# Performance work log

Measured on AMD Instinct MI355X. Metric: run time of the kernel, lower is better.

## Reference

```python
import jax, jax.numpy as jnp
import numpy as np

B, S, H = 2, 2048, 2048
NH, NKV, HD = 16, 4, 128
ROPE_BASE = 10000.0


def rotate_half(x):
    x1, x2 = jnp.split(x, 2, axis=-1)
    return jnp.concatenate((-x2, x1), axis=-1)


def setup_inputs() -> dict:
    key = jax.random.key(0)
    ks = jax.random.split(key, 6)
    hidden_states = jax.random.normal(ks[0], (B, S, H), dtype=jnp.float32)
    # additive causal mask, as used by HF: 0 on allowed, large negative on masked
    causal = jnp.triu(jnp.full((S, S), -1e9, dtype=jnp.float32), k=1)
    attention_mask = jnp.broadcast_to(causal[None, None], (B, 1, S, S))
    position_ids = jnp.broadcast_to(jnp.arange(S, dtype=jnp.int64)[None], (B, S))
    scale = 1.0 / np.sqrt(H)
    Wq = jax.random.normal(ks[1], (NH * HD, H), dtype=jnp.float32) * scale
    Wk = jax.random.normal(ks[2], (NKV * HD, H), dtype=jnp.float32) * scale
    Wv = jax.random.normal(ks[3], (NKV * HD, H), dtype=jnp.float32) * scale
    Wo = jax.random.normal(ks[4], (H, NH * HD), dtype=jnp.float32) * scale
    return {"hidden_states": hidden_states, "attention_mask": attention_mask,
            "position_ids": position_ids, "Wq": Wq, "Wk": Wk, "Wv": Wv, "Wo": Wo}


def reference(hidden_states, attention_mask, position_ids, Wq, Wk, Wv, Wo):
    b, s, _ = hidden_states.shape
    # projections (torch Linear: y = x W^T)
    q = jnp.einsum('bsh,oh->bso', hidden_states, Wq).reshape(b, s, NH, HD).transpose(0, 2, 1, 3)
    k = jnp.einsum('bsh,oh->bso', hidden_states, Wk).reshape(b, s, NKV, HD).transpose(0, 2, 1, 3)
    v = jnp.einsum('bsh,oh->bso', hidden_states, Wv).reshape(b, s, NKV, HD).transpose(0, 2, 1, 3)
    # RoPE
    inv_freq = 1.0 / (ROPE_BASE ** (jnp.arange(0, HD, 2, dtype=jnp.float32) / HD))  # [HD/2]
    freqs = position_ids.astype(jnp.float32)[:, :, None] * inv_freq[None, None, :]  # [B,S,HD/2]
    emb = jnp.concatenate((freqs, freqs), axis=-1)                                  # [B,S,HD]
    cos = jnp.cos(emb)[:, None]  # [B,1,S,HD]
    sin = jnp.sin(emb)[:, None]
    q = q * cos + rotate_half(q) * sin
    k = k * cos + rotate_half(k) * sin
    # GQA repeat (repeat_interleave along head axis)
    n_rep = NH // NKV
    k = jnp.repeat(k, n_rep, axis=1)
    v = jnp.repeat(v, n_rep, axis=1)
    scale = HD ** -0.5
    attn = jnp.einsum('bhqd,bhkd->bhqk', q, k) * scale
    attn = attn + attention_mask
    attn = jax.nn.softmax(attn.astype(jnp.float32), axis=-1).astype(q.dtype)
    out = jnp.einsum('bhqk,bhkd->bhqd', attn, v)            # [B,NH,S,HD]
    out = out.transpose(0, 2, 1, 3).reshape(b, s, NH * HD)  # [B,S,H]
    return jnp.einsum('bso,ho->bsh', out, Wo)
```

## Files before the change

kernel.cpp:

```cpp
#include <hip/hip_runtime.h>


#define B_ 2
#define S_ 2048
#define H_ 2048
#define NH_ 16
#define NKV_ 4
#define HD_ 128
#define QKV_N 3072

typedef unsigned short u16;
typedef unsigned int u32;
typedef unsigned long long u64;
typedef __attribute__((ext_vector_type(8))) short short8;
typedef __attribute__((ext_vector_type(4))) float floatx4;
typedef __attribute__((ext_vector_type(16))) float floatx16;

__device__ __forceinline__ u16 f2bf(float f) {
    union { float f; u32 u; } v; v.f = f;
    u32 u = v.u;
    return (u16)((u + 0x7fffu + ((u >> 16) & 1u)) >> 16);
}
__device__ __forceinline__ float bf2f(u16 h) {
    union { u32 u; float f; } v; v.u = ((u32)h) << 16;
    return v.f;
}
__device__ __forceinline__ void store_out(u16* p, float v)  { *p = f2bf(v); }
__device__ __forceinline__ void store_out(float* p, float v) { *p = v; }

__device__ __forceinline__ void gload_lds16(const void* g, void* l) {
    __builtin_amdgcn_global_load_lds(
        (const __attribute__((address_space(1))) void*)g,
        (__attribute__((address_space(3))) void*)l, 16, 0, 0);
}

__device__ __forceinline__ u32 cvtpk(float lo, float hi) {
    u32 r;
    asm("v_cvt_pk_bf16_f32 %0, %1, %2" : "=v"(r) : "v"(lo), "v"(hi));
    return r;
}

__device__ __forceinline__ void pl32swap(u32& a, u32& b) {
#if __has_builtin(__builtin_amdgcn_permlane32_swap)
    typedef __attribute__((ext_vector_type(2))) int iv2;
    iv2 r = __builtin_amdgcn_permlane32_swap((int)a, (int)b, false, false);
    a = (u32)r[0];
    b = (u32)r[1];
#else
    asm volatile("v_permlane32_swap_b32 %0, %1" : "+v"(a), "+v"(b));
#endif
}

__global__ __launch_bounds__(256) void cast_all(const float* __restrict__ hs,
                                                const float* __restrict__ Wq,
                                                const float* __restrict__ Wk,
                                                const float* __restrict__ Wv,
                                                const float* __restrict__ Wo,
                                                u16* __restrict__ hs_b,
                                                u16* __restrict__ wqkv_b,
                                                u16* __restrict__ wo_b) {
    int q = blockIdx.x * 256 + threadIdx.x;
    const float* src;
    u16* dst;
    if (q < 2097152)      { src = hs; dst = hs_b; }
    else if (q < 3145728) { q -= 2097152; src = Wq; dst = wqkv_b; }
    else if (q < 3407872) { q -= 3145728; src = Wk; dst = wqkv_b + 2048 * 2048; }
    else if (q < 3670016) { q -= 3407872; src = Wv; dst = wqkv_b + 2560 * 2048; }
    else                  { q -= 3670016; src = Wo; dst = wo_b; }
    float4 f = ((const float4*)src)[q];
    u32 lo = ((u32)f2bf(f.y) << 16) | f2bf(f.x);
    u32 hi2 = ((u32)f2bf(f.w) << 16) | f2bf(f.z);
    *(u64*)(dst + (size_t)q * 4) = (u64)lo | ((u64)hi2 << 32);
}

template <typename OutT>
__global__ __launch_bounds__(256) void gemm128(const u16* __restrict__ A,
                                               const u16* __restrict__ Bm,
                                               OutT* __restrict__ C,
                                               int M, int N, int K) {
    __shared__ __align__(16) u16 As[128][32];
    __shared__ __align__(16) u16 Bs[128][32];
    const int tid  = threadIdx.x;
    const int wave = tid >> 6;
    const int lane = tid & 63;
    const int quad = lane >> 4;
    const int l16  = lane & 15;

    const int nbx = gridDim.x, nby = gridDim.y;
    const int total = nbx * nby;
    int n = (int)blockIdx.y * nbx + (int)blockIdx.x;
    if ((total & 7) == 0) {
        int cpx = total >> 3;
        n = (n & 7) * cpx + (n >> 3);
    }
    const int m0 = (n / nbx) * 128;
    const int n0 = (n % nbx) * 128;

    const int wm = (wave >> 1) * 64;
    const int wn = (wave & 1) * 64;
    const int srow = tid >> 2;
    const int scol = (tid & 3) * 8;

    floatx4 acc[4][4] = {};

    for (int k0 = 0; k0 < K; k0 += 32) {
        __syncthreads();
        gload_lds16(A  + (size_t)(m0 + srow) * K + k0 + scol,      &As[srow][scol]);
        gload_lds16(A  + (size_t)(m0 + 64 + srow) * K + k0 + scol, &As[64 + srow][scol]);
        gload_lds16(Bm + (size_t)(n0 + srow) * K + k0 + scol,      &Bs[srow][scol]);
        gload_lds16(Bm + (size_t)(n0 + 64 + srow) * K + k0 + scol, &Bs[64 + srow][scol]);
        __syncthreads();
        short8 af[4], bfv[4];
        for (int i = 0; i < 4; ++i) {
            af[i]  = *(const short8*)&As[wm + i * 16 + l16][quad * 8];
            bfv[i] = *(const short8*)&Bs[wn + i * 16 + l16][quad * 8];
        }
        for (int mi = 0; mi < 4; ++mi)
            for (int ni = 0; ni < 4; ++ni)
                acc[mi][ni] = __builtin_amdgcn_mfma_f32_16x16x32_bf16(
                    af[mi], bfv[ni], acc[mi][ni], 0, 0, 0);
    }
    for (int mi = 0; mi < 4; ++mi)
        for (int ni = 0; ni < 4; ++ni)
            for (int r = 0; r < 4; ++r) {
                int row = m0 + wm + mi * 16 + quad * 4 + r;
                int col = n0 + wn + ni * 16 + l16;
                store_out(C + (size_t)row * N + col, acc[mi][ni][r]);
            }
}

__global__ __launch_bounds__(256) void rope2(u16* buf) {
    int i = blockIdx.x * 256 + threadIdx.x;
    int hofs, nheads;
    float oscale;
    if (i < 4194304) { hofs = 0;    nheads = 16; oscale = 0.08838834764831845f; }
    else             { i -= 4194304; hofs = 2048; nheads = 4;  oscale = 1.0f; }
    int d = i & 63;
    int t = i >> 6;
    int head = t % nheads;
    int row  = t / nheads;
    int s    = row & (S_ - 1);
    size_t base = (size_t)row * QKV_N + hofs + head * HD_;
    float invf = exp2f(-(float)d * (13.28771237954945f / 64.0f));
    float fr = (float)s * invf;
    float sn, cs;
    sincosf(fr, &sn, &cs);
    float x1 = bf2f(buf[base + d]);
    float x2 = bf2f(buf[base + d + 64]);
    buf[base + d]      = f2bf((x1 * cs - x2 * sn) * oscale);
    buf[base + d + 64] = f2bf((x2 * cs + x1 * sn) * oscale);
}

__global__ __launch_bounds__(256) void transpose_v(const u16* __restrict__ qkv,
                                                   u16* __restrict__ vt) {
    __shared__ u16 t[32][33];
    const int tx = threadIdx.x, ty = threadIdx.y;
    const int c0 = blockIdx.x * 32, s0 = blockIdx.y * 32, b = blockIdx.z;
    for (int i = 0; i < 4; ++i)
        t[ty + i * 8][tx] =
            qkv[((size_t)(b * S_ + s0 + ty + i * 8)) * QKV_N + 2560 + c0 + tx];
    __syncthreads();
    for (int i = 0; i < 4; ++i)
        vt[((size_t)(b * 512 + c0 + ty + i * 8)) * S_ + s0 + tx] = t[tx][ty + i * 8];
}

__global__ __launch_bounds__(256) void flash_attn(const u16* __restrict__ qkv,
                                                  const u16* __restrict__ vtg,
                                                  u16* __restrict__ o) {
    __shared__ __align__(16) u16 KsL[64 * 128];
    __shared__ __align__(16) u16 VtL[128 * 64];

    const int tid  = threadIdx.x;
    const int wave = tid >> 6;
    const int lane = tid & 63;
    const int l31  = lane & 31;
    const int hi   = lane >> 5;
    const int wq   = wave >> 1;
    const int kb   = wave & 1;

    const int bx = (int)blockIdx.x;
    const int by = (int)blockIdx.y;
    const int flip = (by >> 3) & 1;
    const int a4 = bx & 15;
    const int jq = flip ? a4 : (31 - a4);
    const int bh = (by & 7) | (((by >> 4) & 1) << 3) | ((bx >> 4) << 4);
    const int b   = bh >> 4;
    const int h   = bh & 15;
    const int kvh = h >> 2;
    const int q0  = jq * 64;

    const size_t qb = ((size_t)(b * S_ + q0 + wq * 32 + l31)) * QKV_N + h * HD_;
    short8 qf[8];
#pragma unroll
    for (int mf = 0; mf < 8; ++mf)
        qf[mf] = *(const short8*)(qkv + qb + mf * 16 + hi * 8);

    floatx16 o_acc[4] = {};
    float l_loc = 0.f;

    const size_t kbase = (size_t)(b * S_) * QKV_N + 2048 + kvh * HD_;
    const size_t vbase = (size_t)((b * NKV_ + kvh) * HD_) * S_;
    const int krow_l = (lane >> 4);
    const int kslot  = lane & 15;
    const int vrow_l = (lane >> 3);
    const int vslot  = lane & 7;

    const int rk = kb * 32 + l31;
    const int kswz = rk & 7;

    for (int kt = 0; kt <= jq; ++kt) {
        __syncthreads();
#pragma unroll
        for (int p = 0; p < 4; ++p) {
            int r = 16 * wave + 4 * p + krow_l;
            gload_lds16(qkv + kbase + (size_t)(kt * 64 + r) * QKV_N
                            + ((kslot ^ (r & 7)) * 8),
                        &KsL[(16 * wave + 4 * p) * 128 + lane * 8]);
            int rv = 32 * wave + 8 * p + vrow_l;
            gload_lds16(vtg + vbase + (size_t)rv * S_ + kt * 64
                            + ((vslot ^ (rv & 7)) * 8),
                        &VtL[(32 * wave + 8 * p) * 64 + lane * 8]);
        }
        __syncthreads();

        floatx16 st = {};
#pragma unroll
        for (int mf = 0; mf < 8; ++mf) {
            short8 kf = *(const short8*)&KsL[rk * 128 + (((mf * 2 + hi) ^ kswz) * 8)];
            st = __builtin_amdgcn_mfma_f32_32x32x16_bf16(kf, qf[mf], st, 0, 0, 0);
        }
        if (kt == jq) {
            int qloc = wq * 32 + l31;
#pragma unroll
            for (int r = 0; r < 16; ++r) {
                int krow = kb * 32 + (r & 3) + 8 * (r >> 2) + 4 * hi;
                if (krow > qloc) st[r] = -INFINITY;
            }
        }
        u32 pk[8];
        float ll = 0.f;
#pragma unroll
        for (int i = 0; i < 8; ++i) {
            float e0 = __expf(st[2 * i]);
            float e1 = __expf(st[2 * i + 1]);
            ll += e0 + e1;
            pk[i] = cvtpk(e0, e1);
        }
        l_loc += ll;
        pl32swap(pk[0], pk[2]);
        pl32swap(pk[1], pk[3]);
        pl32swap(pk[4], pk[6]);
        pl32swap(pk[5], pk[7]);
        union { u32 u[4]; short8 s; } c0, c1;
        c0.u[0] = pk[0]; c0.u[1] = pk[1]; c0.u[2] = pk[2]; c0.u[3] = pk[3];
        c1.u[0] = pk[4]; c1.u[1] = pk[5]; c1.u[2] = pk[6]; c1.u[3] = pk[7];
#pragma unroll
        for (int dblk = 0; dblk < 4; ++dblk) {
            int rv = dblk * 32 + l31;
            int sw = rv & 7;
            short8 va = *(const short8*)&VtL[rv * 64 + (((kb * 4 + hi) ^ sw) * 8)];
            o_acc[dblk] = __builtin_amdgcn_mfma_f32_32x32x16_bf16(va, c0.s, o_acc[dblk], 0, 0, 0);
            short8 vb = *(const short8*)&VtL[rv * 64 + (((kb * 4 + 2 + hi) ^ sw) * 8)];
            o_acc[dblk] = __builtin_amdgcn_mfma_f32_32x32x16_bf16(vb, c1.s, o_acc[dblk], 0, 0, 0);
        }
    }

    float lt = l_loc + __shfl_xor(l_loc, 32, 64);
    __syncthreads();
    float* scr = (float*)KsL;
    if (kb == 1) scr[wq * 64 + lane] = lt;
    __syncthreads();
    float linv = 0.f;
    if (kb == 0) linv = 1.0f / (lt + scr[wq * 64 + lane]);

#pragma unroll
    for (int dblk = 0; dblk < 4; ++dblk) {
        __syncthreads();
        if (kb == 1) {
#pragma unroll
            for (int r = 0; r < 16; ++r)
                scr[wq * 1088 + lane * 17 + r] = o_acc[dblk][r];
        }
        __syncthreads();
        if (kb == 0) {
            const int row = q0 + wq * 32 + l31;
#pragma unroll
            for (int rg = 0; rg < 4; ++rg) {
                float v0 = (o_acc[dblk][rg * 4 + 0] + scr[wq * 1088 + lane * 17 + rg * 4 + 0]) * linv;
                float v1 = (o_acc[dblk][rg * 4 + 1] + scr[wq * 1088 + lane * 17 + rg * 4 + 1]) * linv;
                float v2 = (o_acc[dblk][rg * 4 + 2] + scr[wq * 1088 + lane * 17 + rg * 4 + 2]) * linv;
                float v3 = (o_acc[dblk][rg * 4 + 3] + scr[wq * 1088 + lane * 17 + rg * 4 + 3]) * linv;
                u32 wlo = cvtpk(v0, v1);
                u32 whi = cvtpk(v2, v3);
                int col = h * HD_ + dblk * 32 + rg * 8 + 4 * hi;
                u64 pack = (u64)wlo | ((u64)whi << 32);
                *(u64*)(o + ((size_t)(b * S_ + row)) * H_ + col) = pack;
            }
        }
    }
}

extern "C" void kernel_launch(void* const* d_in, const int* in_sizes, int n_in,
                              void* d_out, int out_size, void* d_ws, size_t ws_size,
                              hipStream_t stream) {
    const float* hs = (const float*)d_in[0];
    const float* Wq = (const float*)d_in[3];
    const float* Wk = (const float*)d_in[4];
    const float* Wv = (const float*)d_in[5];
    const float* Wo = (const float*)d_in[6];

    char* ws = (char*)d_ws;
    const size_t MB = 1024 * 1024;
    u16* hs_b   = (u16*)(ws + 0);
    u16* wqkv_b = (u16*)(ws + 16 * MB);
    u16* vt_b   = (u16*)(ws + 16 * MB);
    u16* wo_b   = (u16*)(ws + 28 * MB);
    u16* qkv    = (u16*)(ws + 36 * MB);

    const int M = B_ * S_;

    cast_all<<<18432, 256, 0, stream>>>(hs, Wq, Wk, Wv, Wo, hs_b, wqkv_b, wo_b);

    gemm128<u16><<<dim3(QKV_N / 128, M / 128), 256, 0, stream>>>(
        hs_b, wqkv_b, qkv, M, QKV_N, H_);

    rope2<<<20480, 256, 0, stream>>>(qkv);

    transpose_v<<<dim3(16, 64, 2), dim3(32, 8), 0, stream>>>(qkv, vt_b);

    flash_attn<<<dim3(32, 32), 256, 0, stream>>>(qkv, vt_b, hs_b);

    gemm128<float><<<dim3(H_ / 128, M / 128), 256, 0, stream>>>(
        hs_b, wo_b, (float*)d_out, M, H_, H_);
}
```

Before: 332.6 us.

## Double the GEMM K-tile and register-prefetch K/V tiles in attention

The GEMM now stages a 64-wide K slice per iteration instead of 32, which halves the number of barrier pairs and gives each wave two MFMA sub-steps per sync. In the attention kernel, K and V tiles are now loaded from global memory into registers one iteration ahead and then written to LDS, replacing the direct global-to-LDS loads. The goal is to overlap global latency with the QK/PV MFMA work. The cost is more LDS in the GEMM and more registers in attention, which may lower occupancy.

```diff
diff --git a/kernel.cpp b/kernel.cpp
--- a/kernel.cpp
+++ b/kernel.cpp
@@ -78,8 +78,8 @@
                                                const u16* __restrict__ Bm,
                                                OutT* __restrict__ C,
                                                int M, int N, int K) {
-    __shared__ __align__(16) u16 As[128][32];
-    __shared__ __align__(16) u16 Bs[128][32];
+    __shared__ __align__(16) u16 As[128][64];
+    __shared__ __align__(16) u16 Bs[128][64];
     const int tid  = threadIdx.x;
     const int wave = tid >> 6;
     const int lane = tid & 63;
@@ -98,30 +98,42 @@
 
     const int wm = (wave >> 1) * 64;
     const int wn = (wave & 1) * 64;
-    const int srow = tid >> 2;
-    const int scol = (tid & 3) * 8;
+    const int srow = tid >> 3;
+    const int scol = (tid & 7) * 8;
 
     floatx4 acc[4][4] = {};
 
-    for (int k0 = 0; k0 < K; k0 += 32) {
-        __syncthreads();
-        gload_lds16(A  + (size_t)(m0 + srow) * K + k0 + scol,      &As[srow][scol]);
-        gload_lds16(A  + (size_t)(m0 + 64 + srow) * K + k0 + scol, &As[64 + srow][scol]);
-        gload_lds16(Bm + (size_t)(n0 + srow) * K + k0 + scol,      &Bs[srow][scol]);
-        gload_lds16(Bm + (size_t)(n0 + 64 + srow) * K + k0 + scol, &Bs[64 + srow][scol]);
-        __syncthreads();
-        short8 af[4], bfv[4];
-        for (int i = 0; i < 4; ++i) {
-            af[i]  = *(const short8*)&As[wm + i * 16 + l16][quad * 8];
-            bfv[i] = *(const short8*)&Bs[wn + i * 16 + l16][quad * 8];
-        }
-        for (int mi = 0; mi < 4; ++mi)
-            for (int ni = 0; ni < 4; ++ni)
-                acc[mi][ni] = __builtin_amdgcn_mfma_f32_16x16x32_bf16(
-                    af[mi], bfv[ni], acc[mi][ni], 0, 0, 0);
-    }
+    for (int k0 = 0; k0 < K; k0 += 64) {
+        __syncthreads();
+#pragma unroll
+        for (int g = 0; g < 4; ++g) {
+            gload_lds16(A  + (size_t)(m0 + g * 32 + srow) * K + k0 + scol,
+                        &As[g * 32 + srow][scol]);
+            gload_lds16(Bm + (size_t)(n0 + g * 32 + srow) * K + k0 + scol,
+                        &Bs[g * 32 + srow][scol]);
+        }
+        __syncthreads();
+#pragma unroll
+        for (int ks = 0; ks < 2; ++ks) {
+            short8 af[4], bfv[4];
+#pragma unroll
+            for (int i = 0; i < 4; ++i) {
+                af[i]  = *(const short8*)&As[wm + i * 16 + l16][ks * 32 + quad * 8];
+                bfv[i] = *(const short8*)&Bs[wn + i * 16 + l16][ks * 32 + quad * 8];
+            }
+#pragma unroll
+            for (int mi = 0; mi < 4; ++mi)
+#pragma unroll
+                for (int ni = 0; ni < 4; ++ni)
+                    acc[mi][ni] = __builtin_amdgcn_mfma_f32_16x16x32_bf16(
+                        af[mi], bfv[ni], acc[mi][ni], 0, 0, 0);
+        }
+    }
+#pragma unroll
     for (int mi = 0; mi < 4; ++mi)
+#pragma unroll
         for (int ni = 0; ni < 4; ++ni)
+#pragma unroll
             for (int r = 0; r < 4; ++r) {
                 int row = m0 + wm + mi * 16 + quad * 4 + r;
                 int col = n0 + wn + ni * 16 + l16;
@@ -204,24 +216,43 @@
     const int kslot  = lane & 15;
     const int vrow_l = (lane >> 3);
     const int vslot  = lane & 7;
+    int kr_[4], kc_[4], vr_[4], vc_[4];
+#pragma unroll
+    for (int p = 0; p < 4; ++p) {
+        kr_[p] = 16 * wave + 4 * p + krow_l;
+        kc_[p] = (kslot ^ (kr_[p] & 7)) * 8;
+        vr_[p] = 32 * wave + 8 * p + vrow_l;
+        vc_[p] = (vslot ^ (vr_[p] & 7)) * 8;
+    }
 
     const int rk = kb * 32 + l31;
     const int kswz = rk & 7;
 
+    short8 kreg[4], vreg[4];
+#pragma unroll
+    for (int p = 0; p < 4; ++p) {
+        kreg[p] = *(const short8*)(qkv + kbase + (size_t)kr_[p] * QKV_N + kc_[p]);
+        vreg[p] = *(const short8*)(vtg + vbase + (size_t)vr_[p] * S_ + vc_[p]);
+    }
+
     for (int kt = 0; kt <= jq; ++kt) {
         __syncthreads();
 #pragma unroll
         for (int p = 0; p < 4; ++p) {
-            int r = 16 * wave + 4 * p + krow_l;
-            gload_lds16(qkv + kbase + (size_t)(kt * 64 + r) * QKV_N
-                            + ((kslot ^ (r & 7)) * 8),
-                        &KsL[(16 * wave + 4 * p) * 128 + lane * 8]);
-            int rv = 32 * wave + 8 * p + vrow_l;
-            gload_lds16(vtg + vbase + (size_t)rv * S_ + kt * 64
-                            + ((vslot ^ (rv & 7)) * 8),
-                        &VtL[(32 * wave + 8 * p) * 64 + lane * 8]);
-        }
-        __syncthreads();
+            *(short8*)&KsL[(16 * wave + 4 * p) * 128 + lane * 8] = kreg[p];
+            *(short8*)&VtL[(32 * wave + 8 * p) * 64 + lane * 8]  = vreg[p];
+        }
+        __syncthreads();
+
+        if (kt < jq) {
+            const size_t ko = kbase + (size_t)((kt + 1) * 64) * QKV_N;
+            const size_t vo = vbase + (size_t)((kt + 1) * 64);
+#pragma unroll
+            for (int p = 0; p < 4; ++p) {
+                kreg[p] = *(const short8*)(qkv + ko + (size_t)kr_[p] * QKV_N + kc_[p]);
+                vreg[p] = *(const short8*)(vtg + vo + (size_t)vr_[p] * S_ + vc_[p]);
+            }
+        }
 
         floatx16 st = {};
 #pragma unroll
```

Result: slower. 367.4 us (+10.5%).

## Register-prefetch next K/V tile in flash attention and fuse rope with V transpose

Applied to the files above, without the earlier changes.

The flash attention loop now loads the next K and V tiles into registers while the current tile is being computed, then writes them to LDS at the start of the next iteration. This replaces the direct global-to-LDS loads and is meant to hide global memory latency behind the MFMA work. Separately, the rope and V-transpose kernels are merged into one launch to save a kernel launch. The merge is safe because the rope blocks only touch the Q and K regions and the transpose blocks only read the V region. The prefetch costs extra registers, which may reduce occupancy.

```diff
diff --git a/kernel.cpp b/kernel.cpp
--- a/kernel.cpp
+++ b/kernel.cpp
@@ -129,39 +129,43 @@
             }
 }
 
-__global__ __launch_bounds__(256) void rope2(u16* buf) {
-    int i = blockIdx.x * 256 + threadIdx.x;
-    int hofs, nheads;
-    float oscale;
-    if (i < 4194304) { hofs = 0;    nheads = 16; oscale = 0.08838834764831845f; }
-    else             { i -= 4194304; hofs = 2048; nheads = 4;  oscale = 1.0f; }
-    int d = i & 63;
-    int t = i >> 6;
-    int head = t % nheads;
-    int row  = t / nheads;
-    int s    = row & (S_ - 1);
-    size_t base = (size_t)row * QKV_N + hofs + head * HD_;
-    float invf = exp2f(-(float)d * (13.28771237954945f / 64.0f));
-    float fr = (float)s * invf;
-    float sn, cs;
-    sincosf(fr, &sn, &cs);
-    float x1 = bf2f(buf[base + d]);
-    float x2 = bf2f(buf[base + d + 64]);
-    buf[base + d]      = f2bf((x1 * cs - x2 * sn) * oscale);
-    buf[base + d + 64] = f2bf((x2 * cs + x1 * sn) * oscale);
-}
-
-__global__ __launch_bounds__(256) void transpose_v(const u16* __restrict__ qkv,
-                                                   u16* __restrict__ vt) {
-    __shared__ u16 t[32][33];
-    const int tx = threadIdx.x, ty = threadIdx.y;
-    const int c0 = blockIdx.x * 32, s0 = blockIdx.y * 32, b = blockIdx.z;
-    for (int i = 0; i < 4; ++i)
-        t[ty + i * 8][tx] =
-            qkv[((size_t)(b * S_ + s0 + ty + i * 8)) * QKV_N + 2560 + c0 + tx];
-    __syncthreads();
-    for (int i = 0; i < 4; ++i)
-        vt[((size_t)(b * 512 + c0 + ty + i * 8)) * S_ + s0 + tx] = t[tx][ty + i * 8];
+__global__ __launch_bounds__(256) void rope_trans(u16* __restrict__ buf,
+                                                  u16* __restrict__ vt) {
+    const int bid = blockIdx.x;
+    const int tid = threadIdx.x;
+    if (bid < 20480) {
+        int i = bid * 256 + tid;
+        int hofs, nheads;
+        float oscale;
+        if (i < 4194304) { hofs = 0;    nheads = 16; oscale = 0.08838834764831845f; }
+        else             { i -= 4194304; hofs = 2048; nheads = 4;  oscale = 1.0f; }
+        int d = i & 63;
+        int t = i >> 6;
+        int head = t % nheads;
+        int row  = t / nheads;
+        int s    = row & (S_ - 1);
+        size_t base = (size_t)row * QKV_N + hofs + head * HD_;
+        float invf = exp2f(-(float)d * (13.28771237954945f / 64.0f));
+        float fr = (float)s * invf;
+        float sn, cs;
+        sincosf(fr, &sn, &cs);
+        float x1 = bf2f(buf[base + d]);
+        float x2 = bf2f(buf[base + d + 64]);
+        buf[base + d]      = f2bf((x1 * cs - x2 * sn) * oscale);
+        buf[base + d + 64] = f2bf((x2 * cs + x1 * sn) * oscale);
+    } else {
+        __shared__ u16 t[32][33];
+        const int b2 = bid - 20480;
+        const int bx = b2 & 15, by = (b2 >> 4) & 63, bz = b2 >> 10;
+        const int tx = tid & 31, ty = tid >> 5;
+        const int c0 = bx * 32, s0 = by * 32, b = bz;
+        for (int i = 0; i < 4; ++i)
+            t[ty + i * 8][tx] =
+                buf[((size_t)(b * S_ + s0 + ty + i * 8)) * QKV_N + 2560 + c0 + tx];
+        __syncthreads();
+        for (int i = 0; i < 4; ++i)
+            vt[((size_t)(b * 512 + c0 + ty + i * 8)) * S_ + s0 + tx] = t[tx][ty + i * 8];
+    }
 }
 
 __global__ __launch_bounds__(256) void flash_attn(const u16* __restrict__ qkv,
@@ -204,24 +208,43 @@
     const int kslot  = lane & 15;
     const int vrow_l = (lane >> 3);
     const int vslot  = lane & 7;
+    int kr_[4], kc_[4], vr_[4], vc_[4];
+#pragma unroll
+    for (int p = 0; p < 4; ++p) {
+        kr_[p] = 16 * wave + 4 * p + krow_l;
+        kc_[p] = (kslot ^ (kr_[p] & 7)) * 8;
+        vr_[p] = 32 * wave + 8 * p + vrow_l;
+        vc_[p] = (vslot ^ (vr_[p] & 7)) * 8;
+    }
 
     const int rk = kb * 32 + l31;
     const int kswz = rk & 7;
 
+    short8 kreg[4], vreg[4];
+#pragma unroll
+    for (int p = 0; p < 4; ++p) {
+        kreg[p] = *(const short8*)(qkv + kbase + (size_t)kr_[p] * QKV_N + kc_[p]);
+        vreg[p] = *(const short8*)(vtg + vbase + (size_t)vr_[p] * S_ + vc_[p]);
+    }
+
     for (int kt = 0; kt <= jq; ++kt) {
         __syncthreads();
 #pragma unroll
         for (int p = 0; p < 4; ++p) {
-            int r = 16 * wave + 4 * p + krow_l;
-            gload_lds16(qkv + kbase + (size_t)(kt * 64 + r) * QKV_N
-                            + ((kslot ^ (r & 7)) * 8),
-                        &KsL[(16 * wave + 4 * p) * 128 + lane * 8]);
-            int rv = 32 * wave + 8 * p + vrow_l;
-            gload_lds16(vtg + vbase + (size_t)rv * S_ + kt * 64
-                            + ((vslot ^ (rv & 7)) * 8),
-                        &VtL[(32 * wave + 8 * p) * 64 + lane * 8]);
-        }
-        __syncthreads();
+            *(short8*)&KsL[(16 * wave + 4 * p) * 128 + lane * 8] = kreg[p];
+            *(short8*)&VtL[(32 * wave + 8 * p) * 64 + lane * 8]  = vreg[p];
+        }
+        __syncthreads();
+
+        if (kt < jq) {
+            const size_t ko = kbase + (size_t)((kt + 1) * 64) * QKV_N;
+            const size_t vo = vbase + (size_t)((kt + 1) * 64);
+#pragma unroll
+            for (int p = 0; p < 4; ++p) {
+                kreg[p] = *(const short8*)(qkv + ko + (size_t)kr_[p] * QKV_N + kc_[p]);
+                vreg[p] = *(const short8*)(vtg + vo + (size_t)vr_[p] * S_ + vc_[p]);
+            }
+        }
 
         floatx16 st = {};
 #pragma unroll
@@ -324,9 +347,7 @@
     gemm128<u16><<<dim3(QKV_N / 128, M / 128), 256, 0, stream>>>(
         hs_b, wqkv_b, qkv, M, QKV_N, H_);
 
-    rope2<<<20480, 256, 0, stream>>>(qkv);
-
-    transpose_v<<<dim3(16, 64, 2), dim3(32, 8), 0, stream>>>(qkv, vt_b);
+    rope_trans<<<22528, 256, 0, stream>>>(qkv, vt_b);
 
     flash_attn<<<dim3(32, 32), 256, 0, stream>>>(qkv, vt_b, hs_b);
 
```

Result: no change. 332.1 us (-0.1%).
